# Performance work log

Hardware: AMD Instinct MI355X
Metric: run time of the kernel (lower is better)

The kernel has to match this reference:

```python
import jax, jax.numpy as jnp
import numpy as np

B, N, D = 8, 2048, 128
NEG = -9.0e15


def setup_inputs() -> dict:
    key = jax.random.key(0)
    ks = jax.random.split(key, 7)
    x = jax.random.normal(ks[0], (B, N, D), dtype=jnp.float32)
    # sparse-ish binary adjacency with self loops, stored dense as float
    adj = (jax.random.uniform(ks[1], (B, N, N)) < 0.1).astype(jnp.float32)
    adj = jnp.maximum(adj, jnp.eye(N, dtype=jnp.float32)[None])
    s = 1.0 / np.sqrt(D)
    W_w = jax.random.uniform(ks[2], (D, D), minval=-s, maxval=s, dtype=jnp.float32)
    W_b = jax.random.uniform(ks[3], (D,), minval=-s, maxval=s, dtype=jnp.float32)
    A = jnp.zeros((D, D), dtype=jnp.float32) + 0.01 * jax.random.normal(ks[4], (D, D), dtype=jnp.float32)
    s2 = 1.0 / np.sqrt(2 * D)
    gate_w = jax.random.uniform(ks[5], (1, 2 * D), minval=-s2, maxval=s2, dtype=jnp.float32)
    gate_b = jax.random.uniform(ks[6], (1,), minval=-s2, maxval=s2, dtype=jnp.float32)
    return {"x": x, "adj": adj, "W_w": W_w, "W_b": W_b, "A": A,
            "gate_w": gate_w, "gate_b": gate_b}


def reference(x, adj, W_w, W_b, A, gate_w, gate_b):
    # h = W(x): [B,N,D]
    h = jnp.einsum('bnf,df->bnd', x, W_w) + W_b
    # e[b,j,k] = (h A)[b,j,:] . h[b,k,:], then symmetrize
    hA = jnp.einsum('bnd,de->bne', h, A)
    e = jnp.einsum('bjl,bkl->bjk', hA, h)
    e = e + jnp.swapaxes(e, 1, 2)
    att = jnp.where(adj > 0, e, jnp.full_like(e, NEG))
    # NOTE: torch code softmaxes over dim=1 (the j axis)
    att = jax.nn.softmax(att, axis=1)
    att = att * adj
    h_prime = jax.nn.relu(jnp.einsum('bij,bjk->bik', att, h))
    gate_in = jnp.concatenate([x, h_prime], axis=-1)  # [B,N,2D]
    coeff = jax.nn.sigmoid(jnp.einsum('bnc,oc->bno', gate_in, gate_w) + gate_b)  # [B,N,1]
    return coeff * x + (1.0 - coeff) * h_prime
```

## Files before the change

### kernel.cpp

```cpp
#include <hip/hip_runtime.h>


#define B_ 8
#define N_ 2048
#define D_ 128

#define BITS_BLOCKS 4096

typedef __attribute__((ext_vector_type(8))) short short8;
typedef __attribute__((ext_vector_type(4))) float f32x4;

#define GLL(gp, lp) __builtin_amdgcn_global_load_lds( \
    (__attribute__((address_space(1))) const unsigned int*)(gp), \
    (__attribute__((address_space(3))) unsigned int*)(lp), 16, 0, 0)

static __device__ __forceinline__ unsigned short f2bf(float f) {
  union { float f; unsigned int u; } v; v.f = f;
  unsigned int r = v.u + 0x7fffu + ((v.u >> 16) & 1u);
  return (unsigned short)(r >> 16);
}
static __device__ __forceinline__ float bf2f(unsigned short u) {
  union { unsigned int u; float f; } v; v.u = ((unsigned int)u) << 16;
  return v.f;
}

#define CAT_OFF  ((size_t)0)
#define VT_OFF   ((size_t)8388608)
#define PUN_OFF  ((size_t)12582912)
#define S_OFF    ((size_t)79691776)
#define WB_OFF   ((size_t)79757312)
#define AT_OFF   ((size_t)79790080)
#define BITS_OFF ((size_t)79822848)

__global__ void k_cvt(const float* __restrict__ W, const float* __restrict__ A,
                      unsigned short* __restrict__ Wb1, unsigned short* __restrict__ Abt) {
  int t = threadIdx.x;
  for (int i = t; i < 128 * 128; i += 256) {
    Wb1[i] = f2bf(W[i]);
    Abt[(i & 127) * 128 + (i >> 7)] = f2bf(A[i]);
  }
}

__global__ __launch_bounds__(256) void kA(const float* __restrict__ adj,
                                          unsigned int* __restrict__ bits,
                                          const float* __restrict__ x,
                                          const unsigned short* __restrict__ Wb1,
                                          const float* __restrict__ Wbias,
                                          const unsigned short* __restrict__ Abt,
                                          unsigned short* __restrict__ cat) {
  __shared__ unsigned short hsm[4][16][136];
  __shared__ unsigned short hasm[4][16][136];
  if (blockIdx.x < BITS_BLOCKS) {
    size_t tid = (size_t)blockIdx.x * 256 + threadIdx.x;
    const float* p = adj + tid * 32;
    unsigned int m = 0;
#pragma unroll
    for (int i = 0; i < 8; i++) {
      f32x4 v = *(const f32x4*)(p + i * 4);
      m |= (v[0] > 0.f ? 1u : 0u) << (i * 4 + 0);
      m |= (v[1] > 0.f ? 1u : 0u) << (i * 4 + 1);
      m |= (v[2] > 0.f ? 1u : 0u) << (i * 4 + 2);
      m |= (v[3] > 0.f ? 1u : 0u) << (i * 4 + 3);
    }
    bits[tid] = m;
    return;
  }
  const int t = threadIdx.x, w = t >> 6, lane = t & 63;
  const int q = lane >> 4, l15 = lane & 15;
  const size_t r0 = (size_t)(blockIdx.x - BITS_BLOCKS) * 64 + w * 16;

  f32x4 acc[8];
#pragma unroll
  for (int dg = 0; dg < 8; dg++) acc[dg] = (f32x4){0.f, 0.f, 0.f, 0.f};
#pragma unroll
  for (int k = 0; k < 4; k++) {
    const float* xp = x + (r0 + l15) * 128 + k * 32 + q * 8;
    f32x4 xa = *(const f32x4*)xp;
    f32x4 xb = *(const f32x4*)(xp + 4);
    short8 af;
#pragma unroll
    for (int e = 0; e < 4; e++) { af[e] = (short)f2bf(xa[e]); af[4 + e] = (short)f2bf(xb[e]); }
#pragma unroll
    for (int dg = 0; dg < 8; dg++) {
      short8 bf = *(const short8*)(Wb1 + (dg * 16 + l15) * 128 + k * 32 + q * 8);
      acc[dg] = __builtin_amdgcn_mfma_f32_16x16x32_bf16(af, bf, acc[dg], 0, 0, 0);
    }
  }
#pragma unroll
  for (int dg = 0; dg < 8; dg++) {
    float bias = Wbias[dg * 16 + l15];
#pragma unroll
    for (int r = 0; r < 4; r++)
      hsm[w][q * 4 + r][dg * 16 + l15] = f2bf(acc[dg][r] + bias);
  }
  __syncthreads();
  f32x4 acc2[8];
#pragma unroll
  for (int dg = 0; dg < 8; dg++) acc2[dg] = (f32x4){0.f, 0.f, 0.f, 0.f};
#pragma unroll
  for (int k = 0; k < 4; k++) {
    short8 af = *(short8*)&hsm[w][l15][k * 32 + q * 8];
#pragma unroll
    for (int dg = 0; dg < 8; dg++) {
      short8 bf = *(const short8*)(Abt + (dg * 16 + l15) * 128 + k * 32 + q * 8);
      acc2[dg] = __builtin_amdgcn_mfma_f32_16x16x32_bf16(af, bf, acc2[dg], 0, 0, 0);
    }
  }
#pragma unroll
  for (int dg = 0; dg < 8; dg++)
#pragma unroll
    for (int r = 0; r < 4; r++)
      hasm[w][q * 4 + r][dg * 16 + l15] = f2bf(acc2[dg][r]);
  __syncthreads();
#pragma unroll
  for (int it = 0; it < 8; it++) {
    int idx = it * 64 + lane;
    int row = idx >> 5, c = idx & 31;
    short8 v = (c < 16) ? *(short8*)&hasm[w][row][c * 8]
                        : *(short8*)&hsm[w][row][(c - 16) * 8];
    *(short8*)(cat + ((r0 + row) << 8) + c * 8) = v;
  }
}

__global__ __launch_bounds__(256, 3) void k2(const unsigned short* __restrict__ cat,
                                             const unsigned int* __restrict__ bits,
                                             unsigned short* __restrict__ pun,
                                             float* __restrict__ s_out) {
  __shared__ unsigned short cj[64 * 256];
  const int t = threadIdx.x, w = t >> 6, lane = t & 63;
  const int q = lane >> 4, l15 = lane & 15;
  const int blk = blockIdx.x;
  const int b = blk & 7;
  const int rest = blk >> 3;
  const int kbase = (rest & 15) * 128;
  const int j0b = (rest >> 4) * 128;
  const size_t bN = (size_t)b * N_;
  const unsigned short* catp = cat + (bN << 8);
  const int kc = kbase + w * 32;
  const int kw = kc >> 5;
  short8 brg[2][8];
#pragma unroll
  for (int p = 0; p < 2; p++) {
    int krow = kc + 2 * l15 + p;
#pragma unroll
    for (int m = 0; m < 8; m++)
      brg[p][m] = *(const short8*)(catp + (((size_t)krow) << 8) +
                                   ((((m * 4 + q) + 16) & 31) * 8));
  }
  float acc0 = 0.f, acc1 = 0.f;
  for (int jt = 0; jt < 2; jt++) {
    const int j0 = j0b + jt * 64;
#pragma unroll
    for (int it = 0; it < 8; it++) {
      int sI = it * 256 + t;
      int row = sI >> 5, c = sI & 31;
      GLL(catp + (((size_t)(j0 + row)) << 8) + (c ^ (row & 7)) * 8,
          (char*)cj + sI * 16);
    }
    __syncthreads();
#pragma unroll
    for (int jsub = 0; jsub < 4; jsub++) {
      const int row = jsub * 16 + l15;
      short8 afr[8];
#pragma unroll
      for (int m = 0; m < 8; m++)
        afr[m] = *(short8*)(cj + row * 256 + (((m * 4 + q) ^ (l15 & 7)) * 8));
      f32x4 e0 = {0.f, 0.f, 0.f, 0.f}, e1 = {0.f, 0.f, 0.f, 0.f};
#pragma unroll
      for (int m = 0; m < 8; m++) {
        e0 = __builtin_amdgcn_mfma_f32_16x16x32_bf16(afr[m], brg[0][m], e0, 0, 0, 0);
        e1 = __builtin_amdgcn_mfma_f32_16x16x32_bf16(afr[m], brg[1][m], e1, 0, 0, 0);
      }
#pragma unroll
      for (int r = 0; r < 4; r++) {
        int jrow = j0 + jsub * 16 + q * 4 + r;
        unsigned int mb = bits[(bN + jrow) * 64 + kw];
        float x0 = ((mb >> (2 * l15)) & 1u) ? __expf(fminf(e0[r], 60.f)) : 0.f;
        float x1 = ((mb >> (2 * l15 + 1)) & 1u) ? __expf(fminf(e1[r], 60.f)) : 0.f;
        acc0 += x0; acc1 += x1;
        unsigned int pk = (unsigned int)f2bf(x0) | ((unsigned int)f2bf(x1) << 16);
        *(unsigned int*)(pun + ((bN + jrow) << 11) + kc + 2 * l15) = pk;
      }
    }
    __syncthreads();
  }
  acc0 += __shfl_xor(acc0, 16, 64); acc0 += __shfl_xor(acc0, 32, 64);
  acc1 += __shfl_xor(acc1, 16, 64); acc1 += __shfl_xor(acc1, 32, 64);
  if (lane < 16) {
    atomicAdd(&s_out[bN + kc + 2 * lane], acc0);
    atomicAdd(&s_out[bN + kc + 2 * lane + 1], acc1);
  }
}

__global__ __launch_bounds__(256) void k1v(const unsigned short* __restrict__ cat,
                                           const float* __restrict__ s,
                                           unsigned short* __restrict__ vt) {
  __shared__ unsigned short tile[64][136];
  __shared__ float rsv[64];
  const int t = threadIdx.x;
  const int blk = blockIdx.x;
  const int b = blk & 7;
  const int nbase = (blk >> 3) * 64;
  if (t < 64) rsv[t] = 1.f / s[(size_t)b * N_ + nbase + t];
#pragma unroll
  for (int k = 0; k < 4; k++) {
    int sI = t + 256 * k;
    int row = sI >> 4, part = sI & 15;
    *(short8*)&tile[row][part * 8] =
        *(const short8*)(cat + (((size_t)(b * N_ + nbase + row)) << 8) + 128 + part * 8);
  }
  __syncthreads();
#pragma unroll
  for (int k = 0; k < 4; k++) {
    int sI = t + 256 * k;
    int dd = sI >> 3, part = sI & 7;
    unsigned short tmp[8];
#pragma unroll
    for (int j = 0; j < 8; j++) {
      int jj = part * 8 + j;
      tmp[j] = f2bf(bf2f(tile[jj][dd]) * rsv[jj]);
    }
    *(short8*)(vt + (((size_t)(b * 128 + dd)) << 11) + nbase + part * 8) = *(short8*)tmp;
  }
}

__global__ __launch_bounds__(256) void k3(const unsigned short* __restrict__ pun,
                                          const unsigned short* __restrict__ vt,
                                          const float* __restrict__ x,
                                          const float* __restrict__ gw,
                                          const float* __restrict__ gb,
                                          float* __restrict__ out) {
  __shared__ char smem[40960];
  const int t = threadIdx.x, w = t >> 6, lane = t & 63;
  const int q = lane >> 4, l15 = lane & 15;
  const int blk = blockIdx.x;
  const int b = blk & 7;
  const int i0 = (blk >> 3) * 32;
  const size_t bN = (size_t)b * N_;
  unsigned short* pa = (unsigned short*)smem;
  unsigned short* vb = (unsigned short*)(smem + 8192);
  const int ph = ((blk >> 3) & 3) * 4;

  f32x4 acc[2][2];
#pragma unroll
  for (int ih = 0; ih < 2; ih++)
#pragma unroll
    for (int dh = 0; dh < 2; dh++) acc[ih][dh] = (f32x4){0.f, 0.f, 0.f, 0.f};

  for (int jt0 = 0; jt0 < N_ / 128; jt0++) {
    const int jt = (jt0 + ph) & (N_ / 128 - 1);
    const int j0 = jt * 128;
#pragma unroll
    for (int it = 0; it < 10; it++) {
      int sI = it * 256 + t;
      const unsigned short* g;
      if (sI < 512) {
        int row = sI >> 4, c = sI & 15;
        g = pun + (((size_t)(bN + i0 + row)) << 11) + j0 + ((c ^ (row & 7)) * 8);
      } else {
        int s2 = sI - 512;
        int dd = s2 >> 4, c = s2 & 15;
        g = vt + (((size_t)(b * 128 + dd)) << 11) + j0 + ((c ^ (dd & 7)) * 8);
      }
      GLL(g, smem + sI * 16);
    }
    __syncthreads();
#pragma unroll
    for (int ks = 0; ks < 4; ks++) {
      short8 af[2], bf[2];
#pragma unroll
      for (int ih = 0; ih < 2; ih++) {
        int m = ih * 16 + l15;
        af[ih] = *(short8*)(pa + m * 128 + (((ks * 4 + q) ^ (m & 7)) * 8));
      }
#pragma unroll
      for (int dh = 0; dh < 2; dh++) {
        int d = w * 32 + dh * 16 + l15;
        bf[dh] = *(short8*)(vb + d * 128 + (((ks * 4 + q) ^ (d & 7)) * 8));
      }
      acc[0][0] = __builtin_amdgcn_mfma_f32_16x16x32_bf16(af[0], bf[0], acc[0][0], 0, 0, 0);
      acc[0][1] = __builtin_amdgcn_mfma_f32_16x16x32_bf16(af[0], bf[1], acc[0][1], 0, 0, 0);
      acc[1][0] = __builtin_amdgcn_mfma_f32_16x16x32_bf16(af[1], bf[0], acc[1][0], 0, 0, 0);
      acc[1][1] = __builtin_amdgcn_mfma_f32_16x16x32_bf16(af[1], bf[1], acc[1][1], 0, 0, 0);
    }
    __syncthreads();
  }
  float* hs = (float*)smem;
  float* co = (float*)(smem + 16896);
#pragma unroll
  for (int ih = 0; ih < 2; ih++)
#pragma unroll
    for (int dh = 0; dh < 2; dh++)
#pragma unroll
      for (int r = 0; r < 4; r++) {
        int row = ih * 16 + q * 4 + r;
        int d = w * 32 + dh * 16 + l15;
        hs[row * 132 + d] = fmaxf(acc[ih][dh][r], 0.f);
      }
  __syncthreads();
  {
    int grow = t >> 3, sub = t & 7;
    const float* xr = x + (((size_t)(bN + i0 + grow)) << 7);
    float z = 0.f;
#pragma unroll
    for (int k = 0; k < 16; k++) {
      int dd = sub + 8 * k;
      z += gw[dd] * xr[dd] + gw[128 + dd] * hs[grow * 132 + dd];
    }
    z += __shfl_xor(z, 1, 64);
    z += __shfl_xor(z, 2, 64);
    z += __shfl_xor(z, 4, 64);
    if (sub == 0) co[grow] = 1.f / (1.f + __expf(-(z + gb[0])));
  }
  __syncthreads();
#pragma unroll
  for (int kk = 0; kk < 4; kk++) {
    int id = kk * 256 + t;
    int row = id >> 5, c4 = id & 31;
    size_t g = (((size_t)(bN + i0 + row)) << 7) + c4 * 4;
    f32x4 xv = *(const f32x4*)(x + g);
    f32x4 hv = *(const f32x4*)(hs + row * 132 + c4 * 4);
    float cf = co[row];
    f32x4 o;
#pragma unroll
    for (int e = 0; e < 4; e++) o[e] = cf * xv[e] + (1.f - cf) * hv[e];
    *(f32x4*)(out + g) = o;
  }
}

extern "C" void kernel_launch(void* const* d_in, const int* in_sizes, int n_in,
                              void* d_out, int out_size, void* d_ws, size_t ws_size,
                              hipStream_t stream) {
  const float* x   = (const float*)d_in[0];
  const float* adj = (const float*)d_in[1];
  const float* Ww  = (const float*)d_in[2];
  const float* Wb  = (const float*)d_in[3];
  const float* A   = (const float*)d_in[4];
  const float* gw  = (const float*)d_in[5];
  const float* gb  = (const float*)d_in[6];
  float* out = (float*)d_out;
  char* ws = (char*)d_ws;

  unsigned short* cat = (unsigned short*)(ws + CAT_OFF);
  unsigned short* vt  = (unsigned short*)(ws + VT_OFF);
  unsigned short* pun = (unsigned short*)(ws + PUN_OFF);
  float* s  = (float*)(ws + S_OFF);
  unsigned short* Wb1 = (unsigned short*)(ws + WB_OFF);
  unsigned short* Abt = (unsigned short*)(ws + AT_OFF);
  unsigned int* bits  = (unsigned int*)(ws + BITS_OFF);

  hipMemsetAsync(s, 0, (size_t)B_ * N_ * sizeof(float), stream);
  k_cvt<<<1, 256, 0, stream>>>(Ww, A, Wb1, Abt);
  kA<<<BITS_BLOCKS + (B_ * N_) / 64, 256, 0, stream>>>(adj, bits, x, Wb1, Wb, Abt, cat);
  k2<<<16 * 16 * B_, 256, 0, stream>>>(cat, bits, pun, s);
  k1v<<<(N_ / 64) * B_, 256, 0, stream>>>(cat, s, vt);
  k3<<<(N_ / 32) * B_, 256, 0, stream>>>(pun, vt, x, gw, gb, out);
}
```

Measured before the change: 309.2 us.

## Double-buffer attention tile in LDS and read V fragments directly from global

In the final aggregation kernel, only the attention-probability tile is staged in shared memory, now double-buffered so the next tile's load overlaps the current tile's MFMAs and one barrier per iteration is dropped. The V operand is read straight from global memory into registers per wave instead of going through LDS. This cuts LDS footprint and sync cost, which may raise occupancy. In exchange, V is fetched by each wave redundantly and without software prefetch, so it depends on cache hits and memory latency.

Result: slower. 323.6 us (+4.6%).

```diff
diff --git a/kernel.cpp b/kernel.cpp
--- a/kernel.cpp
+++ b/kernel.cpp
@@ -230,15 +230,14 @@
                                           const float* __restrict__ gw,
                                           const float* __restrict__ gb,
                                           float* __restrict__ out) {
-  __shared__ char smem[40960];
+  __shared__ char smem[17408];
   const int t = threadIdx.x, w = t >> 6, lane = t & 63;
   const int q = lane >> 4, l15 = lane & 15;
   const int blk = blockIdx.x;
   const int b = blk & 7;
   const int i0 = (blk >> 3) * 32;
   const size_t bN = (size_t)b * N_;
-  unsigned short* pa = (unsigned short*)smem;
-  unsigned short* vb = (unsigned short*)(smem + 8192);
+  const unsigned short* vbase = vt + (((size_t)(b * 128)) << 11);
   const int ph = ((blk >> 3) & 3) * 4;
 
   f32x4 acc[2][2];
@@ -247,24 +246,31 @@
 #pragma unroll
     for (int dh = 0; dh < 2; dh++) acc[ih][dh] = (f32x4){0.f, 0.f, 0.f, 0.f};
 
-  for (int jt0 = 0; jt0 < N_ / 128; jt0++) {
-    const int jt = (jt0 + ph) & (N_ / 128 - 1);
-    const int j0 = jt * 128;
-#pragma unroll
-    for (int it = 0; it < 10; it++) {
+  {
+    const int j0 = (ph & 15) * 128;
+#pragma unroll
+    for (int it = 0; it < 2; it++) {
       int sI = it * 256 + t;
-      const unsigned short* g;
-      if (sI < 512) {
+      int row = sI >> 4, c = sI & 15;
+      GLL(pun + (((size_t)(bN + i0 + row)) << 11) + j0 + ((c ^ (row & 7)) * 8),
+          smem + sI * 16);
+    }
+  }
+  for (int jt0 = 0; jt0 < 16; jt0++) {
+    const int j0 = ((jt0 + ph) & 15) * 128;
+    unsigned short* pa = (unsigned short*)(smem + (jt0 & 1) * 8192);
+    __syncthreads();
+    if (jt0 < 15) {
+      const int j0n = ((jt0 + 1 + ph) & 15) * 128;
+      char* nb = smem + ((jt0 + 1) & 1) * 8192;
+#pragma unroll
+      for (int it = 0; it < 2; it++) {
+        int sI = it * 256 + t;
         int row = sI >> 4, c = sI & 15;
-        g = pun + (((size_t)(bN + i0 + row)) << 11) + j0 + ((c ^ (row & 7)) * 8);
-      } else {
-        int s2 = sI - 512;
-        int dd = s2 >> 4, c = s2 & 15;
-        g = vt + (((size_t)(b * 128 + dd)) << 11) + j0 + ((c ^ (dd & 7)) * 8);
-      }
-      GLL(g, smem + sI * 16);
-    }
-    __syncthreads();
+        GLL(pun + (((size_t)(bN + i0 + row)) << 11) + j0n + ((c ^ (row & 7)) * 8),
+            nb + sI * 16);
+      }
+    }
 #pragma unroll
     for (int ks = 0; ks < 4; ks++) {
       short8 af[2], bf[2];
@@ -276,15 +282,15 @@
 #pragma unroll
       for (int dh = 0; dh < 2; dh++) {
         int d = w * 32 + dh * 16 + l15;
-        bf[dh] = *(short8*)(vb + d * 128 + (((ks * 4 + q) ^ (d & 7)) * 8));
+        bf[dh] = *(const short8*)(vbase + (((size_t)d) << 11) + j0 + (ks * 4 + q) * 8);
       }
       acc[0][0] = __builtin_amdgcn_mfma_f32_16x16x32_bf16(af[0], bf[0], acc[0][0], 0, 0, 0);
       acc[0][1] = __builtin_amdgcn_mfma_f32_16x16x32_bf16(af[0], bf[1], acc[0][1], 0, 0, 0);
       acc[1][0] = __builtin_amdgcn_mfma_f32_16x16x32_bf16(af[1], bf[0], acc[1][0], 0, 0, 0);
       acc[1][1] = __builtin_amdgcn_mfma_f32_16x16x32_bf16(af[1], bf[1], acc[1][1], 0, 0, 0);
     }
-    __syncthreads();
-  }
+  }
+  __syncthreads();
   float* hs = (float*)smem;
   float* co = (float*)(smem + 16896);
 #pragma unroll
```
